# Optimization experiments

Measured on AMD Instinct MI355X. Metric: run time of the kernel, lower is better.

The kernel has to match this reference:

```python
import jax, jax.numpy as jnp
import numpy as np
from jax import lax

# Covers the fully-specified prefix of ColorHead.downgrade (the high-headroom region):
# ColorDownsample(16) -> ModePool2d(11,1,1) -> Conv1x1(3->32) -> depthwise Conv1x1 -> BN -> LeakyReLU
#   -> Conv1x1(32->32) -> depthwise Conv1x1 -> BN -> LeakyReLU

NBINS = 17
KS = 11  # ModePool2d kernel_size
EPS = 1e-5
SLOPE = 0.01  # torch LeakyReLU default negative_slope


def color_downsample(x, down=16.0):
    return jnp.round(x * 255.0 / down) * down / 256.0


def mode_pool2d(x, kernel_size=KS, stride=1, padding=1):
    # Equivalent to torch unfold + scatter_add histogram + argmax, but computes
    # per-bin counts with a windowed sum over one-hot indicators (no giant unfold).
    xp = jnp.pad(x, ((0, 0), (0, 0), (padding, padding), (padding, padding)))
    bins = jnp.clip(jnp.round(xp * 16.0), 0.0, 16.0).astype(jnp.int32)  # [B,C,H,W]
    onehot = (bins[:, :, None, :, :] == jnp.arange(NBINS, dtype=jnp.int32)[None, None, :, None, None]).astype(x.dtype)  # [B,C,17,H,W]
    counts = lax.reduce_window(
        onehot, jnp.array(0, x.dtype), lax.add,
        window_dimensions=(1, 1, 1, kernel_size, kernel_size),
        window_strides=(1, 1, 1, stride, stride),
        padding='VALID')  # [B,C,17,Ho,Wo]
    mode_bins = jnp.argmax(counts, axis=2)  # first max, like torch argmax
    return mode_bins.astype(x.dtype) / 16.0


def conv1x1(x, w, b):
    # w: [O, C], b: [O]
    return jnp.einsum('bchw,oc->bohw', x, w) + b[None, :, None, None]


def dwconv1x1(x, w, b):
    # depthwise 1x1 (groups == channels): per-channel affine. w: [C], b: [C]
    return x * w[None, :, None, None] + b[None, :, None, None]


def batchnorm(x, gamma, beta):
    # training-mode BN: batch statistics over (B,H,W)
    mean = jnp.mean(x, axis=(0, 2, 3), keepdims=True)
    var = jnp.var(x, axis=(0, 2, 3), keepdims=True)
    xn = (x - mean) * lax.rsqrt(var + EPS)
    return xn * gamma[None, :, None, None] + beta[None, :, None, None]


def leaky_relu(x):
    return jnp.where(x >= 0, x, SLOPE * x)


def setup_inputs() -> dict:
    key = jax.random.key(0)
    ks = jax.random.split(key, 8)
    C_in, C_h = 3, 32
    x = jax.random.uniform(ks[0], (8, C_in, 512, 512), dtype=jnp.float32)
    w1 = jax.random.normal(ks[1], (C_h, C_in), dtype=jnp.float32) * 0.1
    b1 = jnp.zeros((C_h,), jnp.float32)
    wd1 = jax.random.normal(ks[2], (C_h,), dtype=jnp.float32) * 0.1 + 1.0
    bd1 = jnp.zeros((C_h,), jnp.float32)
    g1 = jnp.ones((C_h,), jnp.float32)
    be1 = jnp.zeros((C_h,), jnp.float32)
    w2 = jax.random.normal(ks[3], (C_h, C_h), dtype=jnp.float32) * 0.1
    b2 = jnp.zeros((C_h,), jnp.float32)
    wd2 = jax.random.normal(ks[4], (C_h,), dtype=jnp.float32) * 0.1 + 1.0
    bd2 = jnp.zeros((C_h,), jnp.float32)
    g2 = jnp.ones((C_h,), jnp.float32)
    be2 = jnp.zeros((C_h,), jnp.float32)
    return dict(x=x, w1=w1, b1=b1, wd1=wd1, bd1=bd1, g1=g1, be1=be1,
                w2=w2, b2=b2, wd2=wd2, bd2=bd2, g2=g2, be2=be2)


def reference(x, w1, b1, wd1, bd1, g1, be1, w2, b2, wd2, bd2, g2, be2):
    h = color_downsample(x)
    h = mode_pool2d(h)                      # [B,3,504,504]
    h = conv1x1(h, w1, b1)                  # [B,32,504,504]
    h = dwconv1x1(h, wd1, bd1)
    h = leaky_relu(batchnorm(h, g1, be1))
    h = conv1x1(h, w2, b2)
    h = dwconv1x1(h, wd2, bd2)
    h = leaky_relu(batchnorm(h, g2, be2))
    return h
```

## Files before the change

### kernel.cpp

```cpp
#include <hip/hip_runtime.h>
#include <hip/hip_bf16.h>

typedef unsigned char u8;
typedef unsigned short u16;
typedef unsigned int u32;
typedef unsigned long long u64;

#define PP     254016
#define NPIX   2032128
#define NTRIP  4913
#define N_F    2032128.0
#define RROWS  4
#define NRB    126

__device__ __forceinline__ float bf2f(__hip_bfloat16 h){ return __bfloat162float(h); }
__device__ __forceinline__ u32 f2bf(float f){
  u32 u = __float_as_uint(f);
  return ((u + 0x7FFFu + ((u >> 16) & 1u)) >> 16);
}
__device__ __forceinline__ float ldv(const void* p, int i, u32 f){
  return f ? ((const float*)p)[i] : bf2f(((const __hip_bfloat16*)p)[i]);
}

typedef unsigned short us2 __attribute__((ext_vector_type(2)));
__device__ __forceinline__ u32 pkmax(u32 a, u32 b){
  us2 x = __builtin_bit_cast(us2, a);
  us2 y = __builtin_bit_cast(us2, b);
  us2 r = __builtin_elementwise_max(x, y);
  return __builtin_bit_cast(u32, r);
}

__device__ __forceinline__ u32 getbin(const void* x, u32 f, int img, int ch, int pr, int pc){
  if ((u32)(pr-1) < 512u && (u32)(pc-1) < 512u){
    float xv = ldv(x, ((img*3+ch)*512 + (pr-1))*512 + (pc-1), f);
    return (u32)(int)rintf(xv * 255.0f * 0.0625f);
  }
  return 0u;
}
__device__ __forceinline__ u64 bdelta(u32 b){ return (b < 16u) ? (1ull << (b*4)) : 0ull; }

__global__ __launch_bounds__(256) void k_init(const u16* __restrict__ xw, u32* __restrict__ flag,
                                              u32* __restrict__ hist){
  int t = threadIdx.x;
  for (int i=t; i<NTRIP; i+=256) hist[i] = 0u;
  if (t < 64){
    u32 bad = 0;
    for (int i=t; i<1024; i+=64) bad |= (u32)(xw[i] >> 15);
    int anybad = __any((int)bad);
    if (t == 0) *flag = anybad ? 1u : 0u;
  }
}

__global__ __launch_bounds__(512) void k_fused(const void* __restrict__ x, const u32* __restrict__ flag,
                                               u16* __restrict__ triple, u32* __restrict__ hist){
  u32 f = *flag;
  int img = blockIdx.y;
  int r0 = blockIdx.x * RROWS;
  int t = threadIdx.x;
  __shared__ u64 CNT[3][518];
  __shared__ u32 lh[NTRIP];
  for (int i=t; i<NTRIP; i+=512) lh[i] = 0u;

  bool extra = (t < 2);
  int colB = 512 + t;
  u64 v[3] = {0,0,0}, vb[3] = {0,0,0};
  u64 rn[3] = {0,0,0}, rnb[3] = {0,0,0};
  u32 r16[3] = {0,0,0}, r16b[3] = {0,0,0};

  for (int j=0; j<11; j++){
    int pr = r0 + j;
    #pragma unroll
    for (int ch=0; ch<3; ch++){
      u32 b = getbin(x, f, img, ch, pr, t);
      v[ch] += bdelta(b);
      rn[ch] = (rn[ch] << 4) | (u64)(b & 15u);
      r16[ch] = (r16[ch] << 1) | (b >> 4);
    }
    if (extra){
      #pragma unroll
      for (int ch=0; ch<3; ch++){
        u32 b = getbin(x, f, img, ch, pr, colB);
        vb[ch] += bdelta(b);
        rnb[ch] = (rnb[ch] << 4) | (u64)(b & 15u);
        r16b[ch] = (r16b[ch] << 1) | (b >> 4);
      }
    }
  }
  #pragma unroll
  for (int ch=0; ch<3; ch++) CNT[ch][t] = v[ch];
  if (extra){
    #pragma unroll
    for (int ch=0; ch<3; ch++) CNT[ch][colB] = vb[ch];
  }
  __syncthreads();

  for (int i=0; i<RROWS; i++){
    int r = r0 + i;
    if (t < 504){
      u32 m3[3];
      #pragma unroll
      for (int ch=0; ch<3; ch++){
        u64 he = 0, ho = 0;
        #pragma unroll
        for (int dx=0; dx<11; dx++){
          u64 n = CNT[ch][t+dx];
          he += n & 0x0F0F0F0F0F0F0F0Full;
          ho += (n >> 4) & 0x0F0F0F0F0F0F0F0Full;
        }
        u64 T = he + ho;
        u32 T2 = (u32)T + (u32)(T >> 32);
        u32 s = (T2 & 0xFFu) + ((T2>>8)&0xFFu) + ((T2>>16)&0xFFu) + (T2>>24);
        u32 e_lo = (u32)he, e_hi = (u32)(he >> 32);
        u32 o_lo = (u32)ho, o_hi = (u32)(ho >> 32);
        u32 k0 = ((e_lo & 0x00FF00FFu) << 5) | 0x000C0010u;
        u32 k1 = ((e_lo >> 3) & 0x1FE01FE0u) | 0x000A000Eu;
        u32 k2 = ((e_hi & 0x00FF00FFu) << 5) | 0x00040008u;
        u32 k3 = ((e_hi >> 3) & 0x1FE01FE0u) | 0x00020006u;
        u32 k4 = ((o_lo & 0x00FF00FFu) << 5) | 0x000B000Fu;
        u32 k5 = ((o_lo >> 3) & 0x1FE01FE0u) | 0x0009000Du;
        u32 k6 = ((o_hi & 0x00FF00FFu) << 5) | 0x00030007u;
        u32 k7 = ((o_hi >> 3) & 0x1FE01FE0u) | 0x00010005u;
        u32 m = pkmax(pkmax(pkmax(k0,k1), pkmax(k2,k3)), pkmax(pkmax(k4,k5), pkmax(k6,k7)));
        u32 best = m >> 16, blo = m & 0xFFFFu;
        best = best > blo ? best : blo;
        u32 k16 = (121u - s) << 5;
        best = best > k16 ? best : k16;
        m3[ch] = 16u - (best & 31u);
      }
      u32 idx = (m3[0]*17u + m3[1])*17u + m3[2];
      triple[img*PP + r*504 + t] = (u16)idx;
      atomicAdd(&lh[idx], 1u);
    }
    __syncthreads();
    if (i+1 < RROWS){
      #pragma unroll
      for (int ch=0; ch<3; ch++){
        u32 nb = getbin(x, f, img, ch, r+11, t);
        rn[ch] = (rn[ch] << 4) | (u64)(nb & 15u);
        r16[ch] = (r16[ch] << 1) | (nb >> 4);
        u32 ob = (u32)((rn[ch] >> 44) & 15u);
        u32 o16 = (r16[ch] >> 11) & 1u;
        v[ch] += bdelta(nb);
        v[ch] -= o16 ? 0ull : (1ull << (ob*4));
        CNT[ch][t] = v[ch];
      }
      if (extra){
        #pragma unroll
        for (int ch=0; ch<3; ch++){
          u32 nb = getbin(x, f, img, ch, r+11, colB);
          rnb[ch] = (rnb[ch] << 4) | (u64)(nb & 15u);
          r16b[ch] = (r16b[ch] << 1) | (nb >> 4);
          u32 ob = (u32)((rnb[ch] >> 44) & 15u);
          u32 o16 = (r16b[ch] >> 11) & 1u;
          vb[ch] += bdelta(nb);
          vb[ch] -= o16 ? 0ull : (1ull << (ob*4));
          CNT[ch][colB] = vb[ch];
        }
      }
    }
    __syncthreads();
  }
  for (int i=t; i<NTRIP; i+=512){ u32 c = lh[i]; if (c) atomicAdd(&hist[i], c); }
}

__device__ __forceinline__ void compute_P1(const u32* __restrict__ hist,
    const void* w1, const void* b1, const void* wd1, const void* bd1,
    const void* g1, const void* be1, u32 f, float* sP ,
    u32* wred , u32* mom ){
  u32 a0=0,a1=0,a2=0,a3=0,a4=0,a5=0,a6=0,a7=0,a8=0;
  for (int t=threadIdx.x; t<NTRIP; t+=256){
    u32 c = hist[t];
    int m2 = t % 17; int tt = t/17; int m1 = tt % 17; int m0 = tt/17;
    a0 += c*m0; a1 += c*m1; a2 += c*m2;
    a3 += c*m0*m0; a4 += c*m1*m1; a5 += c*m2*m2;
    a6 += c*m0*m1; a7 += c*m0*m2; a8 += c*m1*m2;
  }
  #pragma unroll
  for (int s=1; s<64; s<<=1){
    a0 += __shfl_xor(a0,s); a1 += __shfl_xor(a1,s); a2 += __shfl_xor(a2,s);
    a3 += __shfl_xor(a3,s); a4 += __shfl_xor(a4,s); a5 += __shfl_xor(a5,s);
    a6 += __shfl_xor(a6,s); a7 += __shfl_xor(a7,s); a8 += __shfl_xor(a8,s);
  }
  int wv = threadIdx.x >> 6;
  if ((threadIdx.x & 63) == 0){
    wred[wv*9+0]=a0; wred[wv*9+1]=a1; wred[wv*9+2]=a2; wred[wv*9+3]=a3; wred[wv*9+4]=a4;
    wred[wv*9+5]=a5; wred[wv*9+6]=a6; wred[wv*9+7]=a7; wred[wv*9+8]=a8;
  }
  __syncthreads();
  if (threadIdx.x < 9) mom[threadIdx.x] = wred[threadIdx.x] + wred[9+threadIdx.x] + wred[18+threadIdx.x] + wred[27+threadIdx.x];
  __syncthreads();
  if (threadIdx.x < 32){
    int o = threadIdx.x;
    double wd = ldv(wd1,o,f);
    double q0 = wd*ldv(w1,o*3+0,f), q1 = wd*ldv(w1,o*3+1,f), q2 = wd*ldv(w1,o*3+2,f);
    double qc = wd*ldv(b1,o,f) + ldv(bd1,o,f);
    double S0=mom[0],S1=mom[1],S2=mom[2],S00=mom[3],S11=mom[4],S22=mom[5],S01=mom[6],S02=mom[7],S12=mom[8];
    double lin = (q0*S0 + q1*S1 + q2*S2) * (1.0/16.0);
    double mean = lin/N_F + qc;
    double quad = (q0*q0*S00 + q1*q1*S11 + q2*q2*S22 + 2.0*(q0*q1*S01 + q0*q2*S02 + q1*q2*S12)) * (1.0/256.0);
    double Ev2 = quad/N_F + 2.0*qc*lin/N_F + qc*qc;
    double var = Ev2 - mean*mean;
    double rstd = 1.0 / sqrt(var + 1e-5);
    double A = rstd * ldv(g1,o,f);
    double B = ldv(be1,o,f) - mean*A;
    sP[o]      = (float)(q0*A);
    sP[32+o]   = (float)(q1*A);
    sP[64+o]   = (float)(q2*A);
    sP[96+o]   = (float)(qc*A + B);
  }
  __syncthreads();
}

__global__ __launch_bounds__(256) void k_stats2(const u32* __restrict__ hist,
    const void* w1, const void* b1, const void* wd1, const void* bd1, const void* g1, const void* be1,
    const void* w2, const void* b2, const void* wd2, const void* bd2,
    double* __restrict__ sums2, const u32* __restrict__ flag){
  u32 f = *flag;
  int o = blockIdx.x;
  __shared__ float sP[128];
  __shared__ u32 wred[36], mom[9];
  __shared__ float sw[32];
  compute_P1(hist, w1,b1,wd1,bd1,g1,be1, f, sP, wred, mom);
  for (int i=threadIdx.x;i<32;i+=256) sw[i] = ldv(w2, o*32+i, f);
  __syncthreads();
  float wd = ldv(wd2, o, f);
  float cc = wd * ldv(b2, o, f) + ldv(bd2, o, f);
  double s=0.0, q=0.0;
  for (int t=threadIdx.x; t<NTRIP; t+=256){
    int m2 = t % 17; int tt = t / 17; int m1 = tt % 17; int m0 = tt / 17;
    float f0 = m0*(1.f/16.f), f1 = m1*(1.f/16.f), f2 = m2*(1.f/16.f);
    float dot = 0.f;
    #pragma unroll
    for (int c=0;c<32;c++){
      float u = sP[c]*f0 + sP[32+c]*f1 + sP[64+c]*f2 + sP[96+c];
      float y = (u >= 0.f) ? u : 0.01f*u;
      dot += sw[c]*y;
    }
    float v2 = wd*dot + cc;
    double cn = (double)hist[t];
    s += cn*(double)v2;
    q += cn*(double)v2*(double)v2;
  }
  __shared__ double red[256];
  red[threadIdx.x]=s; __syncthreads();
  for (int off=128; off>0; off>>=1){ if (threadIdx.x<off) red[threadIdx.x]+=red[threadIdx.x+off]; __syncthreads(); }
  if (threadIdx.x==0) sums2[o]=red[0];
  __syncthreads();
  red[threadIdx.x]=q; __syncthreads();
  for (int off=128; off>0; off>>=1){ if (threadIdx.x<off) red[threadIdx.x]+=red[threadIdx.x+off]; __syncthreads(); }
  if (threadIdx.x==0) sums2[32+o]=red[0];
}

__global__ __launch_bounds__(256) void k_lut(const u32* __restrict__ hist, const double* __restrict__ sums2,
    const void* w1, const void* b1, const void* wd1, const void* bd1, const void* g1, const void* be1,
    const void* w2, const void* b2, const void* wd2, const void* bd2,
    const void* g2, const void* be2,
    float* __restrict__ lutf, u32* __restrict__ lutb, const u32* __restrict__ flag){
  u32 f = *flag;
  __shared__ float sP[128];
  __shared__ u32 wred[36], mom[9];
  __shared__ float sw[1024];
  __shared__ float ka[32], kb[32];
  compute_P1(hist, w1,b1,wd1,bd1,g1,be1, f, sP, wred, mom);
  for (int i=threadIdx.x;i<1024;i+=256) sw[i]=ldv(w2, i, f);
  if (threadIdx.x < 32){
    int o = threadIdx.x;
    double mean = sums2[o] / N_F;
    double var  = sums2[32+o] / N_F - mean*mean;
    double rstd = 1.0 / sqrt(var + 1e-5);
    double A = rstd * (double)ldv(g2, o, f);
    double B = (double)ldv(be2, o, f) - mean*A;
    double wd = (double)ldv(wd2, o, f);
    ka[o] = (float)(wd*A);
    kb[o] = (float)((wd*(double)ldv(b2, o, f) + (double)ldv(bd2, o, f))*A + B);
  }
  __syncthreads();
  int t = blockIdx.x*256 + threadIdx.x;
  if (t >= NTRIP) return;
  int m2 = t % 17; int tt = t/17; int m1 = tt % 17; int m0 = tt/17;
  float f0=m0*(1.f/16.f), f1=m1*(1.f/16.f), f2=m2*(1.f/16.f);
  float y1[32];
  #pragma unroll
  for (int c=0;c<32;c++){
    float u = sP[c]*f0 + sP[32+c]*f1 + sP[64+c]*f2 + sP[96+c];
    y1[c] = (u>=0.f)?u:0.01f*u;
  }
  float y2[32];
  #pragma unroll
  for (int o=0;o<32;o++){
    float dot=0.f;
    #pragma unroll
    for (int c=0;c<32;c++) dot += sw[o*32+c]*y1[c];
    float v = dot*ka[o] + kb[o];
    y2[o] = (v>=0.f)?v:0.01f*v;
    lutf[t*32+o] = y2[o];
  }
  #pragma unroll
  for (int j=0;j<16;j++)
    lutb[t*16+j] = f2bf(y2[2*j]) | (f2bf(y2[2*j+1]) << 16);
}

__global__ __launch_bounds__(256) void k_out(const u16* __restrict__ triple, const float* __restrict__ lutf,
                                             const u32* __restrict__ lutb,
                                             void* __restrict__ out, const u32* __restrict__ flag){
  u32 f = *flag;
  int g = blockIdx.x*256 + threadIdx.x;
  if (g >= NPIX/2) return;
  int p0 = g*2;
  int bimg = p0 / PP; int pix = p0 - bimg*PP;
  u32 tt = *(const u32*)(triple + p0);
  u32 ia = tt & 0xFFFFu, ib = tt >> 16;
  if (f){
    const float4* La = (const float4*)(lutf + (size_t)ia*32);
    const float4* Lb = (const float4*)(lutf + (size_t)ib*32);
    float* ob = (float*)out + (size_t)bimg*32*PP + pix;
    #pragma unroll
    for (int j=0;j<8;j++){
      float4 a = La[j]; float4 b = Lb[j];
      float2 v;
      v.x=a.x; v.y=b.x; *(float2*)(ob + (size_t)(4*j+0)*PP) = v;
      v.x=a.y; v.y=b.y; *(float2*)(ob + (size_t)(4*j+1)*PP) = v;
      v.x=a.z; v.y=b.z; *(float2*)(ob + (size_t)(4*j+2)*PP) = v;
      v.x=a.w; v.y=b.w; *(float2*)(ob + (size_t)(4*j+3)*PP) = v;
    }
  } else {
    const uint4* La = (const uint4*)(lutb + (size_t)ia*16);
    const uint4* Lb = (const uint4*)(lutb + (size_t)ib*16);
    u16* ob = (u16*)out + (size_t)bimg*32*PP + pix;
    #pragma unroll
    for (int j=0;j<4;j++){
      uint4 A = La[j]; uint4 B = Lb[j];
      *(u32*)(ob + (size_t)(8*j+0)*PP) = __builtin_amdgcn_perm(B.x, A.x, 0x05040100u);
      *(u32*)(ob + (size_t)(8*j+1)*PP) = __builtin_amdgcn_perm(B.x, A.x, 0x07060302u);
      *(u32*)(ob + (size_t)(8*j+2)*PP) = __builtin_amdgcn_perm(B.y, A.y, 0x05040100u);
      *(u32*)(ob + (size_t)(8*j+3)*PP) = __builtin_amdgcn_perm(B.y, A.y, 0x07060302u);
      *(u32*)(ob + (size_t)(8*j+4)*PP) = __builtin_amdgcn_perm(B.z, A.z, 0x05040100u);
      *(u32*)(ob + (size_t)(8*j+5)*PP) = __builtin_amdgcn_perm(B.z, A.z, 0x07060302u);
      *(u32*)(ob + (size_t)(8*j+6)*PP) = __builtin_amdgcn_perm(B.w, A.w, 0x05040100u);
      *(u32*)(ob + (size_t)(8*j+7)*PP) = __builtin_amdgcn_perm(B.w, A.w, 0x07060302u);
    }
  }
}

extern "C" void kernel_launch(void* const* d_in, const int* in_sizes, int n_in,
                              void* d_out, int out_size, void* d_ws, size_t ws_size,
                              hipStream_t stream){
  const void* x   = d_in[0];
  const void* w1  = d_in[1];
  const void* b1  = d_in[2];
  const void* wd1 = d_in[3];
  const void* bd1 = d_in[4];
  const void* g1  = d_in[5];
  const void* be1 = d_in[6];
  const void* w2  = d_in[7];
  const void* b2  = d_in[8];
  const void* wd2 = d_in[9];
  const void* bd2 = d_in[10];
  const void* g2  = d_in[11];
  const void* be2 = d_in[12];

  char* w = (char*)d_ws;
  auto alloc = [&](size_t bytes)->char* { char* p = w; w += (bytes + 255) & ~(size_t)255; return p; };
  u32*   flag   = (u32*)  alloc(256);
  u16*   triple = (u16*)  alloc(2ull*NPIX);
  u32*   hist   = (u32*)  alloc(4ull*NTRIP);
  double* sums2 = (double*)alloc(64ull*8);
  float* lutf   = (float*)alloc(4ull*NTRIP*32);
  u32*   lutb   = (u32*)  alloc(4ull*NTRIP*16);

  k_init<<<dim3(1), 256, 0, stream>>>((const u16*)x, flag, hist);
  k_fused<<<dim3(NRB, 8), 512, 0, stream>>>(x, flag, triple, hist);
  k_stats2<<<dim3(32), 256, 0, stream>>>(hist, w1,b1,wd1,bd1,g1,be1, w2,b2,wd2,bd2, sums2, flag);
  k_lut<<<dim3((NTRIP+255)/256), 256, 0, stream>>>(hist, sums2, w1,b1,wd1,bd1,g1,be1,
                                                   w2,b2,wd2,bd2, g2,be2, lutf, lutb, flag);
  k_out<<<dim3((NPIX/2)/256), 256, 0, stream>>>(triple, lutf, lutb, d_out, flag);
}
```

Baseline: 385.2 us.

## Merge stats and LUT kernels, apply BN2 in output kernel, pre-split counts

Merges the second-layer stats kernel and the LUT kernel into one wider-grid kernel. It writes pre-BN values into a LUT and accumulates sums with double atomics, so the final BN2 affine and LeakyReLU are applied in the output kernel. It also stores the column counts already split into even and odd nibble lanes as 128-bit entries, which removes the masking from the 11-tap horizontal sum. It doubles the rows per block in the mode-pool kernel. The costs are more shared memory, extra FMA and activation work per output element, and bf16 output now being converted per pixel instead of read from a packed LUT.

```diff
diff --git a/kernel.cpp b/kernel.cpp
--- a/kernel.cpp
+++ b/kernel.cpp
@@ -10,8 +10,8 @@
 #define NPIX   2032128
 #define NTRIP  4913
 #define N_F    2032128.0
-#define RROWS  4
-#define NRB    126
+#define RROWS  8
+#define NRB    63
 
 __device__ __forceinline__ float bf2f(__hip_bfloat16 h){ return __bfloat162float(h); }
 __device__ __forceinline__ u32 f2bf(float f){
@@ -40,9 +40,10 @@
 __device__ __forceinline__ u64 bdelta(u32 b){ return (b < 16u) ? (1ull << (b*4)) : 0ull; }
 
 __global__ __launch_bounds__(256) void k_init(const u16* __restrict__ xw, u32* __restrict__ flag,
-                                              u32* __restrict__ hist){
+                                              u32* __restrict__ hist, u32* __restrict__ s2){
   int t = threadIdx.x;
   for (int i=t; i<NTRIP; i+=256) hist[i] = 0u;
+  if (t < 128) s2[t] = 0u;
   if (t < 64){
     u32 bad = 0;
     for (int i=t; i<1024; i+=64) bad |= (u32)(xw[i] >> 15);
@@ -57,10 +58,11 @@
   int img = blockIdx.y;
   int r0 = blockIdx.x * RROWS;
   int t = threadIdx.x;
-  __shared__ u64 CNT[3][518];
+  __shared__ ulonglong2 CNT[3][516];
   __shared__ u32 lh[NTRIP];
   for (int i=t; i<NTRIP; i+=512) lh[i] = 0u;
 
+  const u64 M4 = 0x0F0F0F0F0F0F0F0Full;
   bool extra = (t < 2);
   int colB = 512 + t;
   u64 v[3] = {0,0,0}, vb[3] = {0,0,0};
@@ -87,10 +89,14 @@
     }
   }
   #pragma unroll
-  for (int ch=0; ch<3; ch++) CNT[ch][t] = v[ch];
+  for (int ch=0; ch<3; ch++){
+    ulonglong2 e; e.x = v[ch] & M4; e.y = (v[ch] >> 4) & M4; CNT[ch][t] = e;
+  }
   if (extra){
     #pragma unroll
-    for (int ch=0; ch<3; ch++) CNT[ch][colB] = vb[ch];
+    for (int ch=0; ch<3; ch++){
+      ulonglong2 e; e.x = vb[ch] & M4; e.y = (vb[ch] >> 4) & M4; CNT[ch][colB] = e;
+    }
   }
   __syncthreads();
 
@@ -103,9 +109,9 @@
         u64 he = 0, ho = 0;
         #pragma unroll
         for (int dx=0; dx<11; dx++){
-          u64 n = CNT[ch][t+dx];
-          he += n & 0x0F0F0F0F0F0F0F0Full;
-          ho += (n >> 4) & 0x0F0F0F0F0F0F0F0Full;
+          ulonglong2 n = CNT[ch][t+dx];
+          he += n.x;
+          ho += n.y;
         }
         u64 T = he + ho;
         u32 T2 = (u32)T + (u32)(T >> 32);
@@ -142,7 +148,7 @@
         u32 o16 = (r16[ch] >> 11) & 1u;
         v[ch] += bdelta(nb);
         v[ch] -= o16 ? 0ull : (1ull << (ob*4));
-        CNT[ch][t] = v[ch];
+        ulonglong2 e; e.x = v[ch] & M4; e.y = (v[ch] >> 4) & M4; CNT[ch][t] = e;
       }
       if (extra){
         #pragma unroll
@@ -154,7 +160,7 @@
           u32 o16 = (r16b[ch] >> 11) & 1u;
           vb[ch] += bdelta(nb);
           vb[ch] -= o16 ? 0ull : (1ull << (ob*4));
-          CNT[ch][colB] = vb[ch];
+          ulonglong2 e; e.x = vb[ch] & M4; e.y = (vb[ch] >> 4) & M4; CNT[ch][colB] = e;
         }
       }
     }
@@ -211,133 +217,125 @@
   __syncthreads();
 }
 
-__global__ __launch_bounds__(256) void k_stats2(const u32* __restrict__ hist,
+__global__ __launch_bounds__(256) void k_stats(const u32* __restrict__ hist,
     const void* w1, const void* b1, const void* wd1, const void* bd1, const void* g1, const void* be1,
     const void* w2, const void* b2, const void* wd2, const void* bd2,
-    double* __restrict__ sums2, const u32* __restrict__ flag){
-  u32 f = *flag;
-  int o = blockIdx.x;
-  __shared__ float sP[128];
-  __shared__ u32 wred[36], mom[9];
-  __shared__ float sw[32];
-  compute_P1(hist, w1,b1,wd1,bd1,g1,be1, f, sP, wred, mom);
-  for (int i=threadIdx.x;i<32;i+=256) sw[i] = ldv(w2, o*32+i, f);
-  __syncthreads();
-  float wd = ldv(wd2, o, f);
-  float cc = wd * ldv(b2, o, f) + ldv(bd2, o, f);
-  double s=0.0, q=0.0;
-  for (int t=threadIdx.x; t<NTRIP; t+=256){
-    int m2 = t % 17; int tt = t / 17; int m1 = tt % 17; int m0 = tt / 17;
-    float f0 = m0*(1.f/16.f), f1 = m1*(1.f/16.f), f2 = m2*(1.f/16.f);
-    float dot = 0.f;
-    #pragma unroll
-    for (int c=0;c<32;c++){
-      float u = sP[c]*f0 + sP[32+c]*f1 + sP[64+c]*f2 + sP[96+c];
-      float y = (u >= 0.f) ? u : 0.01f*u;
-      dot += sw[c]*y;
-    }
-    float v2 = wd*dot + cc;
-    double cn = (double)hist[t];
-    s += cn*(double)v2;
-    q += cn*(double)v2*(double)v2;
-  }
-  __shared__ double red[256];
-  red[threadIdx.x]=s; __syncthreads();
-  for (int off=128; off>0; off>>=1){ if (threadIdx.x<off) red[threadIdx.x]+=red[threadIdx.x+off]; __syncthreads(); }
-  if (threadIdx.x==0) sums2[o]=red[0];
-  __syncthreads();
-  red[threadIdx.x]=q; __syncthreads();
-  for (int off=128; off>0; off>>=1){ if (threadIdx.x<off) red[threadIdx.x]+=red[threadIdx.x+off]; __syncthreads(); }
-  if (threadIdx.x==0) sums2[32+o]=red[0];
-}
-
-__global__ __launch_bounds__(256) void k_lut(const u32* __restrict__ hist, const double* __restrict__ sums2,
-    const void* w1, const void* b1, const void* wd1, const void* bd1, const void* g1, const void* be1,
-    const void* w2, const void* b2, const void* wd2, const void* bd2,
-    const void* g2, const void* be2,
-    float* __restrict__ lutf, u32* __restrict__ lutb, const u32* __restrict__ flag){
+    float* __restrict__ lutpre, double* __restrict__ sums2, const u32* __restrict__ flag){
   u32 f = *flag;
   __shared__ float sP[128];
   __shared__ u32 wred[36], mom[9];
   __shared__ float sw[1024];
+  __shared__ float swd[32], scc[32];
+  compute_P1(hist, w1,b1,wd1,bd1,g1,be1, f, sP, wred, mom);
+  for (int i=threadIdx.x;i<1024;i+=256) sw[i] = ldv(w2, i, f);
+  if (threadIdx.x < 32){
+    int o = threadIdx.x;
+    float wd = ldv(wd2,o,f);
+    swd[o] = wd;
+    scc[o] = wd*ldv(b2,o,f) + ldv(bd2,o,f);
+  }
+  __syncthreads();
+  int o = threadIdx.x & 31, slot = threadIdx.x >> 5;
+  double s = 0.0, q = 0.0;
+  for (int t = blockIdx.x*8 + slot; t < NTRIP; t += gridDim.x*8){
+    int m2 = t % 17; int tt = t/17; int m1 = tt % 17; int m0 = tt/17;
+    float f0 = m0*(1.f/16.f), f1 = m1*(1.f/16.f), f2v = m2*(1.f/16.f);
+    float dot = 0.f;
+    #pragma unroll
+    for (int c=0;c<32;c++){
+      float u = sP[c]*f0 + sP[32+c]*f1 + sP[64+c]*f2v + sP[96+c];
+      float y = (u >= 0.f) ? u : 0.01f*u;
+      dot += sw[o*32+c]*y;
+    }
+    float v2 = swd[o]*dot + scc[o];
+    lutpre[t*32+o] = v2;
+    double cn = (double)hist[t];
+    s += cn*(double)v2;
+    q += cn*(double)v2*(double)v2;
+  }
+  s += __shfl_xor(s, 32);
+  q += __shfl_xor(q, 32);
+  __shared__ double sred[2][4][32];
+  int wv = threadIdx.x >> 6, ln = threadIdx.x & 63;
+  if (ln < 32){ sred[0][wv][ln] = s; sred[1][wv][ln] = q; }
+  __syncthreads();
+  if (threadIdx.x < 32){
+    int oo = threadIdx.x;
+    double ss = sred[0][0][oo]+sred[0][1][oo]+sred[0][2][oo]+sred[0][3][oo];
+    atomicAdd(&sums2[oo], ss);
+  } else if (threadIdx.x < 64){
+    int oo = threadIdx.x - 32;
+    double qq = sred[1][0][oo]+sred[1][1][oo]+sred[1][2][oo]+sred[1][3][oo];
+    atomicAdd(&sums2[32+oo], qq);
+  }
+}
+
+__global__ __launch_bounds__(256) void k_out(const u16* __restrict__ triple, const float* __restrict__ lutpre,
+                                             const double* __restrict__ sums2,
+                                             const void* g2, const void* be2,
+                                             void* __restrict__ out, const u32* __restrict__ flag){
+  u32 f = *flag;
   __shared__ float ka[32], kb[32];
-  compute_P1(hist, w1,b1,wd1,bd1,g1,be1, f, sP, wred, mom);
-  for (int i=threadIdx.x;i<1024;i+=256) sw[i]=ldv(w2, i, f);
   if (threadIdx.x < 32){
     int o = threadIdx.x;
     double mean = sums2[o] / N_F;
     double var  = sums2[32+o] / N_F - mean*mean;
     double rstd = 1.0 / sqrt(var + 1e-5);
-    double A = rstd * (double)ldv(g2, o, f);
-    double B = (double)ldv(be2, o, f) - mean*A;
-    double wd = (double)ldv(wd2, o, f);
-    ka[o] = (float)(wd*A);
-    kb[o] = (float)((wd*(double)ldv(b2, o, f) + (double)ldv(bd2, o, f))*A + B);
-  }
-  __syncthreads();
-  int t = blockIdx.x*256 + threadIdx.x;
-  if (t >= NTRIP) return;
-  int m2 = t % 17; int tt = t/17; int m1 = tt % 17; int m0 = tt/17;
-  float f0=m0*(1.f/16.f), f1=m1*(1.f/16.f), f2=m2*(1.f/16.f);
-  float y1[32];
-  #pragma unroll
-  for (int c=0;c<32;c++){
-    float u = sP[c]*f0 + sP[32+c]*f1 + sP[64+c]*f2 + sP[96+c];
-    y1[c] = (u>=0.f)?u:0.01f*u;
-  }
-  float y2[32];
-  #pragma unroll
-  for (int o=0;o<32;o++){
-    float dot=0.f;
-    #pragma unroll
-    for (int c=0;c<32;c++) dot += sw[o*32+c]*y1[c];
-    float v = dot*ka[o] + kb[o];
-    y2[o] = (v>=0.f)?v:0.01f*v;
-    lutf[t*32+o] = y2[o];
-  }
-  #pragma unroll
-  for (int j=0;j<16;j++)
-    lutb[t*16+j] = f2bf(y2[2*j]) | (f2bf(y2[2*j+1]) << 16);
-}
-
-__global__ __launch_bounds__(256) void k_out(const u16* __restrict__ triple, const float* __restrict__ lutf,
-                                             const u32* __restrict__ lutb,
-                                             void* __restrict__ out, const u32* __restrict__ flag){
-  u32 f = *flag;
+    double A = rstd * (double)ldv(g2,o,f);
+    double B = (double)ldv(be2,o,f) - mean*A;
+    ka[o] = (float)A; kb[o] = (float)B;
+  }
+  __syncthreads();
   int g = blockIdx.x*256 + threadIdx.x;
   if (g >= NPIX/2) return;
   int p0 = g*2;
   int bimg = p0 / PP; int pix = p0 - bimg*PP;
   u32 tt = *(const u32*)(triple + p0);
   u32 ia = tt & 0xFFFFu, ib = tt >> 16;
+  const float4* La = (const float4*)(lutpre + (size_t)ia*32);
+  const float4* Lb = (const float4*)(lutpre + (size_t)ib*32);
   if (f){
-    const float4* La = (const float4*)(lutf + (size_t)ia*32);
-    const float4* Lb = (const float4*)(lutf + (size_t)ib*32);
     float* ob = (float*)out + (size_t)bimg*32*PP + pix;
     #pragma unroll
     for (int j=0;j<8;j++){
       float4 a = La[j]; float4 b = Lb[j];
+      float4 K = *(const float4*)&ka[4*j];
+      float4 C = *(const float4*)&kb[4*j];
       float2 v;
-      v.x=a.x; v.y=b.x; *(float2*)(ob + (size_t)(4*j+0)*PP) = v;
-      v.x=a.y; v.y=b.y; *(float2*)(ob + (size_t)(4*j+1)*PP) = v;
-      v.x=a.z; v.y=b.z; *(float2*)(ob + (size_t)(4*j+2)*PP) = v;
-      v.x=a.w; v.y=b.w; *(float2*)(ob + (size_t)(4*j+3)*PP) = v;
+      float ax, bx;
+      ax = fmaf(a.x, K.x, C.x); ax = ax>=0.f?ax:0.01f*ax;
+      bx = fmaf(b.x, K.x, C.x); bx = bx>=0.f?bx:0.01f*bx;
+      v.x=ax; v.y=bx; *(float2*)(ob + (size_t)(4*j+0)*PP) = v;
+      ax = fmaf(a.y, K.y, C.y); ax = ax>=0.f?ax:0.01f*ax;
+      bx = fmaf(b.y, K.y, C.y); bx = bx>=0.f?bx:0.01f*bx;
+      v.x=ax; v.y=bx; *(float2*)(ob + (size_t)(4*j+1)*PP) = v;
+      ax = fmaf(a.z, K.z, C.z); ax = ax>=0.f?ax:0.01f*ax;
+      bx = fmaf(b.z, K.z, C.z); bx = bx>=0.f?bx:0.01f*bx;
+      v.x=ax; v.y=bx; *(float2*)(ob + (size_t)(4*j+2)*PP) = v;
+      ax = fmaf(a.w, K.w, C.w); ax = ax>=0.f?ax:0.01f*ax;
+      bx = fmaf(b.w, K.w, C.w); bx = bx>=0.f?bx:0.01f*bx;
+      v.x=ax; v.y=bx; *(float2*)(ob + (size_t)(4*j+3)*PP) = v;
     }
   } else {
-    const uint4* La = (const uint4*)(lutb + (size_t)ia*16);
-    const uint4* Lb = (const uint4*)(lutb + (size_t)ib*16);
     u16* ob = (u16*)out + (size_t)bimg*32*PP + pix;
     #pragma unroll
-    for (int j=0;j<4;j++){
-      uint4 A = La[j]; uint4 B = Lb[j];
-      *(u32*)(ob + (size_t)(8*j+0)*PP) = __builtin_amdgcn_perm(B.x, A.x, 0x05040100u);
-      *(u32*)(ob + (size_t)(8*j+1)*PP) = __builtin_amdgcn_perm(B.x, A.x, 0x07060302u);
-      *(u32*)(ob + (size_t)(8*j+2)*PP) = __builtin_amdgcn_perm(B.y, A.y, 0x05040100u);
-      *(u32*)(ob + (size_t)(8*j+3)*PP) = __builtin_amdgcn_perm(B.y, A.y, 0x07060302u);
-      *(u32*)(ob + (size_t)(8*j+4)*PP) = __builtin_amdgcn_perm(B.z, A.z, 0x05040100u);
-      *(u32*)(ob + (size_t)(8*j+5)*PP) = __builtin_amdgcn_perm(B.z, A.z, 0x07060302u);
-      *(u32*)(ob + (size_t)(8*j+6)*PP) = __builtin_amdgcn_perm(B.w, A.w, 0x05040100u);
-      *(u32*)(ob + (size_t)(8*j+7)*PP) = __builtin_amdgcn_perm(B.w, A.w, 0x07060302u);
+    for (int j=0;j<8;j++){
+      float4 a = La[j]; float4 b = Lb[j];
+      float4 K = *(const float4*)&ka[4*j];
+      float4 C = *(const float4*)&kb[4*j];
+      float ax, bx;
+      ax = fmaf(a.x, K.x, C.x); ax = ax>=0.f?ax:0.01f*ax;
+      bx = fmaf(b.x, K.x, C.x); bx = bx>=0.f?bx:0.01f*bx;
+      *(u32*)(ob + (size_t)(4*j+0)*PP) = f2bf(ax) | (f2bf(bx) << 16);
+      ax = fmaf(a.y, K.y, C.y); ax = ax>=0.f?ax:0.01f*ax;
+      bx = fmaf(b.y, K.y, C.y); bx = bx>=0.f?bx:0.01f*bx;
+      *(u32*)(ob + (size_t)(4*j+1)*PP) = f2bf(ax) | (f2bf(bx) << 16);
+      ax = fmaf(a.z, K.z, C.z); ax = ax>=0.f?ax:0.01f*ax;
+      bx = fmaf(b.z, K.z, C.z); bx = bx>=0.f?bx:0.01f*bx;
+      *(u32*)(ob + (size_t)(4*j+2)*PP) = f2bf(ax) | (f2bf(bx) << 16);
+      ax = fmaf(a.w, K.w, C.w); ax = ax>=0.f?ax:0.01f*ax;
+      bx = fmaf(b.w, K.w, C.w); bx = bx>=0.f?bx:0.01f*bx;
+      *(u32*)(ob + (size_t)(4*j+3)*PP) = f2bf(ax) | (f2bf(bx) << 16);
     }
   }
 }
@@ -361,17 +359,15 @@
 
   char* w = (char*)d_ws;
   auto alloc = [&](size_t bytes)->char* { char* p = w; w += (bytes + 255) & ~(size_t)255; return p; };
-  u32*   flag   = (u32*)  alloc(256);
-  u16*   triple = (u16*)  alloc(2ull*NPIX);
-  u32*   hist   = (u32*)  alloc(4ull*NTRIP);
-  double* sums2 = (double*)alloc(64ull*8);
-  float* lutf   = (float*)alloc(4ull*NTRIP*32);
-  u32*   lutb   = (u32*)  alloc(4ull*NTRIP*16);
-
-  k_init<<<dim3(1), 256, 0, stream>>>((const u16*)x, flag, hist);
+  u32*    flag   = (u32*)   alloc(256);
+  u16*    triple = (u16*)   alloc(2ull*NPIX);
+  u32*    hist   = (u32*)   alloc(4ull*NTRIP);
+  double* sums2  = (double*)alloc(64ull*8);
+  float*  lutpre = (float*) alloc(4ull*NTRIP*32);
+
+  k_init<<<dim3(1), 256, 0, stream>>>((const u16*)x, flag, hist, (u32*)sums2);
   k_fused<<<dim3(NRB, 8), 512, 0, stream>>>(x, flag, triple, hist);
-  k_stats2<<<dim3(32), 256, 0, stream>>>(hist, w1,b1,wd1,bd1,g1,be1, w2,b2,wd2,bd2, sums2, flag);
-  k_lut<<<dim3((NTRIP+255)/256), 256, 0, stream>>>(hist, sums2, w1,b1,wd1,bd1,g1,be1,
-                                                   w2,b2,wd2,bd2, g2,be2, lutf, lutb, flag);
-  k_out<<<dim3((NPIX/2)/256), 256, 0, stream>>>(triple, lutf, lutb, d_out, flag);
-}
+  k_stats<<<dim3(256), 256, 0, stream>>>(hist, w1,b1,wd1,bd1,g1,be1, w2,b2,wd2,bd2,
+                                         lutpre, sums2, flag);
+  k_out<<<dim3((NPIX/2)/256), 256, 0, stream>>>(triple, lutpre, sums2, g2, be2, d_out, flag);
+}
```

Result: faster. 372.5 us (-3.3%).
